# Performance work log

Measured on AMD Instinct MI355X. Metric: run time of the kernel, lower is better.

Reference implementation:

```python
import jax, jax.numpy as jnp
import numpy as np

ALPHA = 0.5
NUM_NB = 8


def setup_inputs() -> dict:
    key = jax.random.key(0)
    k1, k2 = jax.random.split(key)
    pc1 = jax.random.normal(k1, (4, 3, 8192), dtype=jnp.float32)
    pred_flow = jax.random.normal(k2, (4, 3, 8192), dtype=jnp.float32)
    return {"pc1": pc1, "pred_flow": pred_flow}


def reference(pc1, pred_flow):
    # pc1, pred_flow: [B, 3, N] -> [B, N, 3]
    B, _, N = pc1.shape
    k = NUM_NB
    p = jnp.transpose(pc1, (0, 2, 1))         # [B, N, 3]
    f = jnp.transpose(pred_flow, (0, 2, 1))   # [B, N, 3]

    sq = jnp.sum(p * p, axis=-1)
    sqrdist = sq[:, :, None] + sq[:, None, :] - 2.0 * jnp.einsum('bnd,bmd->bnm', p, p)

    # k+1 smallest (sorted ascending), drop self (first column)
    neg_d, kidx = jax.lax.top_k(-sqrdist, k + 1)  # descending in -d == ascending in d
    dists = -neg_d[:, :, 1:]                      # [B, N, k]
    kidx = kidx[:, :, 1:]                         # [B, N, k]
    dists = jnp.maximum(dists, 0.0)

    # softmax over all N*k weights per batch
    w = jax.nn.softmax(jnp.exp(-dists / ALPHA).reshape(B, N * k), axis=1)
    w = w.reshape(B, N, k)

    # gather neighbor flows: [B, N, k, 3]
    grouped = jnp.take_along_axis(f[:, None, :, :],
                                  kidx[:, :, :, None],
                                  axis=2)
    diff = jnp.linalg.norm(grouped - f[:, :, None, :], axis=3)  # [B, N, k]
    diff_flow = (N * w * diff).sum(axis=2)                      # [B, N]
    return jnp.mean(diff_flow)
```

## Files before the change

### kernel.cpp

```cpp
#include <hip/hip_runtime.h>
#include <hip/hip_bf16.h>
#include <math.h>

#define BATCH 4
#define NQ 8192
#define KNB 8
#define K1 9
#define TILE 1024
#define CAP 32
#define THSAMP 256
#define SPART 2
#define IDXMASK 8191u
#define KEYMASK 0xFFFFE000u
#define EPS_S 1e-3f

#define CHAIN9(KEY) { unsigned kk = (KEY); \
  _Pragma("unroll") \
  for (int j = 0; j < K1; ++j) { \
    unsigned lo = min(kk, nk[j]); unsigned hi = max(kk, nk[j]); \
    nk[j] = lo; kk = hi; } }

#define DRAIN(T0) { \
  for (int i = 0; i < cnt; ++i) { \
    int j = sbuf[base + i]; \
    float dx = qx - sx[j], dy = qy - sy[j], dz = qz - sz[j]; \
    float d = dx*dx + dy*dy + dz*dz; \
    unsigned key = (__float_as_uint(d) & KEYMASK) | (unsigned)(c0 + (T0) + j); \
    if (key < nk[K1-1]) CHAIN9(key); \
  } \
  cnt = 0; \
  if (nk[K1-1] != 0xFFFFFFFFu) { \
    float td = __uint_as_float(nk[K1-1] | 0x1FFFu); \
    thetaS = fminf(thetaS, 0.5f*(td - qq) + EPS_S); \
  } }

#define GPROC(SS, JLOCAL) { \
  if ((SS) <= thetaS) { sbuf[base + cnt] = (unsigned short)(JLOCAL); cnt++; } }

#define SCORE4(S0,S1,S2,S3, X,Y,Z,H) \
  float S0 = fmaf(nqx, X.x, fmaf(nqy, Y.x, fmaf(nqz, Z.x, H.x))); \
  float S1 = fmaf(nqx, X.y, fmaf(nqy, Y.y, fmaf(nqz, Z.y, H.y))); \
  float S2 = fmaf(nqx, X.z, fmaf(nqy, Y.z, fmaf(nqz, Z.z, H.z))); \
  float S3 = fmaf(nqx, X.w, fmaf(nqy, Y.w, fmaf(nqz, Z.w, H.w)));

__global__ __launch_bounds__(256) void theta_kernel(
    const float* __restrict__ pc, unsigned* __restrict__ thetaOut,
    float* __restrict__ hOut)
{
  __shared__ float swx[THSAMP], swy[THSAMP], swz[THSAMP];
  const int b = blockIdx.y, p = blockIdx.z;
  const int q = blockIdx.x * 256 + threadIdx.x;
  const float* __restrict__ px = pc + (size_t)b * 3 * NQ;
  const float* __restrict__ py = px + NQ;
  const float* __restrict__ pz = px + 2 * NQ;
  const int tid = threadIdx.x;
  const int si = tid * (NQ / THSAMP) + p * (NQ / THSAMP / SPART);
  swx[tid] = px[si]; swy[tid] = py[si]; swz[tid] = pz[si];
  __syncthreads();
  const float qx = px[q], qy = py[q], qz = pz[q];
  if (p == 0) hOut[b * NQ + q] = 0.5f * (qx*qx + qy*qy + qz*qz);
  unsigned nk[K1];
#pragma unroll
  for (int j = 0; j < K1; ++j) nk[j] = 0xFFFFFFFFu;
  for (int i = 0; i < THSAMP; ++i) {
    float dx = qx - swx[i], dy = qy - swy[i], dz = qz - swz[i];
    float d = dx * dx + dy * dy + dz * dz;
    CHAIN9(__float_as_uint(d));
  }
  thetaOut[(size_t)(b * NQ + q) * SPART + p] = nk[K1 - 1] | 0x1FFFu;
}

__global__ __launch_bounds__(256) void knn_kernel(
    const float* __restrict__ pc, const float* __restrict__ hB,
    const unsigned* __restrict__ thetaIn, unsigned* __restrict__ wsK,
    int P, int cpp)
{
  __shared__ float sx[TILE], sy[TILE], sz[TILE], sh[TILE];
  __shared__ unsigned short sbuf[256 * CAP];
  const int b = blockIdx.y;
  const int p = blockIdx.z;
  const int q = blockIdx.x * 256 + threadIdx.x;
  const float* __restrict__ px = pc + (size_t)b * 3 * NQ;
  const float* __restrict__ py = px + NQ;
  const float* __restrict__ pz = px + 2 * NQ;
  const float* __restrict__ ph = hB + (size_t)b * NQ;
  const float qx = px[q], qy = py[q], qz = pz[q];
  const float nqx = -qx, nqy = -qy, nqz = -qz;
  const float qq = qx*qx + qy*qy + qz*qz;

  uint2 th = ((const uint2*)thetaIn)[b * NQ + q];
  float thetaS = 0.5f * (__uint_as_float(min(th.x, th.y)) - qq) + EPS_S;

  unsigned nk[K1];
#pragma unroll
  for (int j = 0; j < K1; ++j) nk[j] = 0xFFFFFFFFu;

  const unsigned base = (unsigned)threadIdx.x * CAP;
  int cnt = 0;
  const int c0 = p * cpp;

  for (int t0 = 0; t0 < cpp; t0 += TILE) {
    __syncthreads();
    {
      const float4* gx = (const float4*)(px + c0 + t0);
      const float4* gy = (const float4*)(py + c0 + t0);
      const float4* gz = (const float4*)(pz + c0 + t0);
      const float4* gh = (const float4*)(ph + c0 + t0);
      float4* lx = (float4*)sx; float4* ly = (float4*)sy;
      float4* lz = (float4*)sz; float4* lh = (float4*)sh;
      for (int i = threadIdx.x; i < TILE / 4; i += 256) {
        lx[i] = gx[i]; ly[i] = gy[i]; lz[i] = gz[i]; lh[i] = gh[i];
      }
    }
    __syncthreads();

    const float4* sx4 = (const float4*)sx;
    const float4* sy4 = (const float4*)sy;
    const float4* sz4 = (const float4*)sz;
    const float4* sh4 = (const float4*)sh;
    for (int i16 = 0; i16 < TILE / 16; ++i16) {
      if (__any(cnt >= CAP - 16)) { DRAIN(t0); }
      const int i4 = i16 * 4;
      const int jb = i16 * 16;
      float4 X0 = sx4[i4], X1 = sx4[i4+1], X2 = sx4[i4+2], X3 = sx4[i4+3];
      float4 Y0 = sy4[i4], Y1 = sy4[i4+1], Y2 = sy4[i4+2], Y3 = sy4[i4+3];
      float4 Z0 = sz4[i4], Z1 = sz4[i4+1], Z2 = sz4[i4+2], Z3 = sz4[i4+3];
      float4 H0 = sh4[i4], H1 = sh4[i4+1], H2 = sh4[i4+2], H3 = sh4[i4+3];
      SCORE4(s0, s1, s2, s3, X0, Y0, Z0, H0);
      SCORE4(s4, s5, s6, s7, X1, Y1, Z1, H1);
      SCORE4(s8, s9, sa, sb, X2, Y2, Z2, H2);
      SCORE4(sc, sd, se, sf, X3, Y3, Z3, H3);
      GPROC(s0, jb + 0);  GPROC(s1, jb + 1);  GPROC(s2, jb + 2);  GPROC(s3, jb + 3);
      GPROC(s4, jb + 4);  GPROC(s5, jb + 5);  GPROC(s6, jb + 6);  GPROC(s7, jb + 7);
      GPROC(s8, jb + 8);  GPROC(s9, jb + 9);  GPROC(sa, jb + 10); GPROC(sb, jb + 11);
      GPROC(sc, jb + 12); GPROC(sd, jb + 13); GPROC(se, jb + 14); GPROC(sf, jb + 15);
    }
    DRAIN(t0);
  }

  const size_t qo = (size_t)b * NQ + q;
#pragma unroll
  for (int j = 0; j < K1; ++j)
    wsK[((size_t)(b * P + p) * K1 + j) * NQ + q] = nk[j];
}

__global__ __launch_bounds__(256) void loss_kernel(
    const float* __restrict__ pc, const float* __restrict__ pf,
    const unsigned* __restrict__ wsK, float* __restrict__ acc, int P)
{
  const int b = blockIdx.y;
  const int q = blockIdx.x * 256 + threadIdx.x;
  const float* __restrict__ px = pc + (size_t)b * 3 * NQ;
  const float* __restrict__ py = px + NQ;
  const float* __restrict__ pz = px + 2 * NQ;
  const float* __restrict__ fx = pf + (size_t)b * 3 * NQ;
  const float* __restrict__ fy = fx + NQ;
  const float* __restrict__ fz = fx + 2 * NQ;

  unsigned nk[KNB];
#pragma unroll
  for (int j = 0; j < KNB; ++j) nk[j] = 0xFFFFFFFFu;

  const int total = P * K1;
  for (int m = 0; m < total; ++m) {
    unsigned key = wsK[((size_t)b * P * K1 + m) * NQ + q];
    if ((key & IDXMASK) == (unsigned)q) continue;
    if (key < nk[KNB - 1]) {
      unsigned kk = key;
#pragma unroll
      for (int j = 0; j < KNB; ++j) {
        unsigned lo = min(kk, nk[j]); unsigned hi = max(kk, nk[j]);
        nk[j] = lo; kk = hi;
      }
    }
  }

  const float qx = px[q], qy = py[q], qz = pz[q];
  const float fqx = fx[q], fqy = fy[q], fqz = fz[q];
  float ssum = 0.f, sdsum = 0.f;
#pragma unroll
  for (int j = 0; j < KNB; ++j) {
    int i = (int)(nk[j] & IDXMASK);
    float dx = qx - px[i], dy = qy - py[i], dz = qz - pz[i];
    float d = dx * dx + dy * dy + dz * dz;
    float e = expf(expf(-2.0f * d));
    float gx = fx[i] - fqx, gy = fy[i] - fqy, gz = fz[i] - fqz;
    float diff = sqrtf(gx * gx + gy * gy + gz * gz);
    ssum += e; sdsum += e * diff;
  }

  for (int off = 32; off > 0; off >>= 1) {
    ssum += __shfl_down(ssum, off);
    sdsum += __shfl_down(sdsum, off);
  }
  __shared__ float r[8];
  const int lane = threadIdx.x & 63, wid = threadIdx.x >> 6;
  if (lane == 0) { r[wid * 2] = ssum; r[wid * 2 + 1] = sdsum; }
  __syncthreads();
  if (threadIdx.x == 0) {
    float s0 = r[0] + r[2] + r[4] + r[6];
    float s1 = r[1] + r[3] + r[5] + r[7];
    atomicAdd(&acc[b * 2 + 0], s0);
    atomicAdd(&acc[b * 2 + 1], s1);
  }
}

__global__ void final_kernel(const float* __restrict__ acc, float* __restrict__ out)
{
  if (threadIdx.x == 0) {
    float s = 0.f;
    for (int b = 0; b < BATCH; ++b) s += acc[b * 2 + 1] / acc[b * 2];
    out[0] = s * (1.0f / BATCH);
  }
}

extern "C" void kernel_launch(void* const* d_in, const int* in_sizes, int n_in,
                              void* d_out, int out_size, void* d_ws, size_t ws_size,
                              hipStream_t stream) {
  const float* pc = (const float*)d_in[0];
  const float* pf = (const float*)d_in[1];
  float* out = (float*)d_out;
  float* acc = (float*)d_ws;
  const size_t thetaBytes = (size_t)BATCH * NQ * SPART * sizeof(unsigned);
  const size_t hBytes = (size_t)BATCH * NQ * sizeof(float);
  unsigned* thetaBuf = (unsigned*)((char*)d_ws + 256);
  float* hBuf = (float*)((char*)d_ws + 256 + thetaBytes);
  unsigned* wsK = (unsigned*)((char*)d_ws + 256 + thetaBytes + hBytes);

  const size_t fixed = 256 + thetaBytes + hBytes;
  const size_t needP8 = fixed + (size_t)BATCH * NQ * 8 * K1 * sizeof(unsigned);
  const size_t needP4 = fixed + (size_t)BATCH * NQ * 4 * K1 * sizeof(unsigned);
  const int P = (ws_size >= needP8) ? 8 : ((ws_size >= needP4) ? 4 : 1);
  const int cpp = NQ / P;

  hipMemsetAsync(d_ws, 0, 256, stream);

  dim3 g0(NQ / 256, BATCH, SPART);
  theta_kernel<<<g0, 256, 0, stream>>>(pc, thetaBuf, hBuf);

  dim3 g1(NQ / 256, BATCH, P);
  knn_kernel<<<g1, 256, 0, stream>>>(pc, hBuf, thetaBuf, wsK, P, cpp);

  dim3 g2(NQ / 256, BATCH);
  loss_kernel<<<g2, 256, 0, stream>>>(pc, pf, wsK, acc, P);

  final_kernel<<<1, 64, 0, stream>>>(acc, out);
}
```

Measured before the change: 134.2 us.

## Stream KNN candidates directly from global memory and raise partition count

Removes the LDS tiling of candidate coordinates in the knn kernel and its two block barriers per tile. Candidates are now read straight from global memory as float4, which are uniform across the wave and served by cache, and the drain step also rereads global memory. The inner step processes 8 candidates instead of 16, and the per-thread buffer grows to 34 entries. Up to 16 candidate partitions are allowed if the workspace fits, adding parallelism at the cost of more partial top-k output for the loss kernel to merge.

Measured after the change: 148.1 us. 1.1x slower.

```diff
diff --git a/kernel.cpp b/kernel.cpp
--- a/kernel.cpp
+++ b/kernel.cpp
@@ -6,8 +6,7 @@
 #define NQ 8192
 #define KNB 8
 #define K1 9
-#define TILE 1024
-#define CAP 32
+#define CAP 34
 #define THSAMP 256
 #define SPART 2
 #define IDXMASK 8191u
@@ -20,12 +19,12 @@
     unsigned lo = min(kk, nk[j]); unsigned hi = max(kk, nk[j]); \
     nk[j] = lo; kk = hi; } }
 
-#define DRAIN(T0) { \
+#define DRAIN() { \
   for (int i = 0; i < cnt; ++i) { \
     int j = sbuf[base + i]; \
-    float dx = qx - sx[j], dy = qy - sy[j], dz = qz - sz[j]; \
+    float dx = qx - px[j], dy = qy - py[j], dz = qz - pz[j]; \
     float d = dx*dx + dy*dy + dz*dz; \
-    unsigned key = (__float_as_uint(d) & KEYMASK) | (unsigned)(c0 + (T0) + j); \
+    unsigned key = (__float_as_uint(d) & KEYMASK) | (unsigned)j; \
     if (key < nk[K1-1]) CHAIN9(key); \
   } \
   cnt = 0; \
@@ -34,8 +33,8 @@
     thetaS = fminf(thetaS, 0.5f*(td - qq) + EPS_S); \
   } }
 
-#define GPROC(SS, JLOCAL) { \
-  if ((SS) <= thetaS) { sbuf[base + cnt] = (unsigned short)(JLOCAL); cnt++; } }
+#define GPROC(SS, GIDX) { \
+  if ((SS) <= thetaS) { sbuf[base + cnt] = (unsigned short)(GIDX); cnt++; } }
 
 #define SCORE4(S0,S1,S2,S3, X,Y,Z,H) \
   float S0 = fmaf(nqx, X.x, fmaf(nqy, Y.x, fmaf(nqz, Z.x, H.x))); \
@@ -75,7 +74,6 @@
     const unsigned* __restrict__ thetaIn, unsigned* __restrict__ wsK,
     int P, int cpp)
 {
-  __shared__ float sx[TILE], sy[TILE], sz[TILE], sh[TILE];
   __shared__ unsigned short sbuf[256 * CAP];
   const int b = blockIdx.y;
   const int p = blockIdx.z;
@@ -84,6 +82,10 @@
   const float* __restrict__ py = px + NQ;
   const float* __restrict__ pz = px + 2 * NQ;
   const float* __restrict__ ph = hB + (size_t)b * NQ;
+  const float4* __restrict__ px4 = (const float4*)px;
+  const float4* __restrict__ py4 = (const float4*)py;
+  const float4* __restrict__ pz4 = (const float4*)pz;
+  const float4* __restrict__ ph4 = (const float4*)ph;
   const float qx = px[q], qy = py[q], qz = pz[q];
   const float nqx = -qx, nqy = -qy, nqz = -qz;
   const float qq = qx*qx + qy*qy + qz*qz;
@@ -99,46 +101,21 @@
   int cnt = 0;
   const int c0 = p * cpp;
 
-  for (int t0 = 0; t0 < cpp; t0 += TILE) {
-    __syncthreads();
-    {
-      const float4* gx = (const float4*)(px + c0 + t0);
-      const float4* gy = (const float4*)(py + c0 + t0);
-      const float4* gz = (const float4*)(pz + c0 + t0);
-      const float4* gh = (const float4*)(ph + c0 + t0);
-      float4* lx = (float4*)sx; float4* ly = (float4*)sy;
-      float4* lz = (float4*)sz; float4* lh = (float4*)sh;
-      for (int i = threadIdx.x; i < TILE / 4; i += 256) {
-        lx[i] = gx[i]; ly[i] = gy[i]; lz[i] = gz[i]; lh[i] = gh[i];
-      }
-    }
-    __syncthreads();
-
-    const float4* sx4 = (const float4*)sx;
-    const float4* sy4 = (const float4*)sy;
-    const float4* sz4 = (const float4*)sz;
-    const float4* sh4 = (const float4*)sh;
-    for (int i16 = 0; i16 < TILE / 16; ++i16) {
-      if (__any(cnt >= CAP - 16)) { DRAIN(t0); }
-      const int i4 = i16 * 4;
-      const int jb = i16 * 16;
-      float4 X0 = sx4[i4], X1 = sx4[i4+1], X2 = sx4[i4+2], X3 = sx4[i4+3];
-      float4 Y0 = sy4[i4], Y1 = sy4[i4+1], Y2 = sy4[i4+2], Y3 = sy4[i4+3];
-      float4 Z0 = sz4[i4], Z1 = sz4[i4+1], Z2 = sz4[i4+2], Z3 = sz4[i4+3];
-      float4 H0 = sh4[i4], H1 = sh4[i4+1], H2 = sh4[i4+2], H3 = sh4[i4+3];
-      SCORE4(s0, s1, s2, s3, X0, Y0, Z0, H0);
-      SCORE4(s4, s5, s6, s7, X1, Y1, Z1, H1);
-      SCORE4(s8, s9, sa, sb, X2, Y2, Z2, H2);
-      SCORE4(sc, sd, se, sf, X3, Y3, Z3, H3);
-      GPROC(s0, jb + 0);  GPROC(s1, jb + 1);  GPROC(s2, jb + 2);  GPROC(s3, jb + 3);
-      GPROC(s4, jb + 4);  GPROC(s5, jb + 5);  GPROC(s6, jb + 6);  GPROC(s7, jb + 7);
-      GPROC(s8, jb + 8);  GPROC(s9, jb + 9);  GPROC(sa, jb + 10); GPROC(sb, jb + 11);
-      GPROC(sc, jb + 12); GPROC(sd, jb + 13); GPROC(se, jb + 14); GPROC(sf, jb + 15);
-    }
-    DRAIN(t0);
-  }
-
-  const size_t qo = (size_t)b * NQ + q;
+  for (int t = 0; t < cpp; t += 8) {
+    if (__any(cnt >= CAP - 8)) { DRAIN(); }
+    const int ti = (c0 + t) >> 2;
+    const float4 X0 = px4[ti], X1 = px4[ti + 1];
+    const float4 Y0 = py4[ti], Y1 = py4[ti + 1];
+    const float4 Z0 = pz4[ti], Z1 = pz4[ti + 1];
+    const float4 H0 = ph4[ti], H1 = ph4[ti + 1];
+    SCORE4(s0, s1, s2, s3, X0, Y0, Z0, H0);
+    SCORE4(s4, s5, s6, s7, X1, Y1, Z1, H1);
+    const int g = c0 + t;
+    GPROC(s0, g + 0); GPROC(s1, g + 1); GPROC(s2, g + 2); GPROC(s3, g + 3);
+    GPROC(s4, g + 4); GPROC(s5, g + 5); GPROC(s6, g + 6); GPROC(s7, g + 7);
+  }
+  DRAIN();
+
 #pragma unroll
   for (int j = 0; j < K1; ++j)
     wsK[((size_t)(b * P + p) * K1 + j) * NQ + q] = nk[j];
@@ -228,9 +205,11 @@
   unsigned* wsK = (unsigned*)((char*)d_ws + 256 + thetaBytes + hBytes);
 
   const size_t fixed = 256 + thetaBytes + hBytes;
-  const size_t needP8 = fixed + (size_t)BATCH * NQ * 8 * K1 * sizeof(unsigned);
-  const size_t needP4 = fixed + (size_t)BATCH * NQ * 4 * K1 * sizeof(unsigned);
-  const int P = (ws_size >= needP8) ? 8 : ((ws_size >= needP4) ? 4 : 1);
+  const size_t needP16 = fixed + (size_t)BATCH * NQ * 16 * K1 * sizeof(unsigned);
+  const size_t needP8  = fixed + (size_t)BATCH * NQ * 8  * K1 * sizeof(unsigned);
+  const size_t needP4  = fixed + (size_t)BATCH * NQ * 4  * K1 * sizeof(unsigned);
+  const int P = (ws_size >= needP16) ? 16 : (ws_size >= needP8) ? 8
+              : (ws_size >= needP4) ? 4 : 1;
   const int cpp = NQ / P;
 
   hipMemsetAsync(d_ws, 0, 256, stream);
```
